# Kernel optimization log

Hardware: AMD Instinct MI355X
Metric: run time of the kernel (lower is better)

Reference implementation:

```python
import jax, jax.numpy as jnp
import numpy as np

N, C, H, W = 4, 256, 32, 32
NH = 2                      # att_nhead
HD = C // NH                # 128 per-head dim
MAX_DIS = 7
WS = 2 * MAX_DIS + 1        # 15 window side
WW = WS * WS                # 225 window positions
T = (C / NH) ** 0.5


def _gather_idx(h, w):
    # idx[wpos, m]: flat index into zero-padded (h+14, w+14) grid of the
    # neighbor at window offset wpos for query pixel m (== F.unfold semantics)
    pw = w + 2 * MAX_DIS
    dy, dx = np.meshgrid(np.arange(WS), np.arange(WS), indexing='ij')
    ys, xs = np.meshgrid(np.arange(h), np.arange(w), indexing='ij')
    idx = (dy.reshape(-1, 1) + ys.reshape(1, -1)) * pw + (dx.reshape(-1, 1) + xs.reshape(1, -1))
    return jnp.asarray(idx, dtype=jnp.int32)  # [WW, h*w]


def setup_inputs() -> dict:
    key = jax.random.key(0)
    ks = jax.random.split(key, 14)
    s = 0.02
    return {
        'q': jax.random.normal(ks[0], (N, C, H, W), jnp.float32),
        'k': jax.random.normal(ks[1], (N, C, H, W), jnp.float32),
        'v': jax.random.normal(ks[2], (N, C, H, W), jnp.float32),
        'Wq': jax.random.normal(ks[3], (C, C), jnp.float32) * s,
        'bq': jnp.zeros((C,), jnp.float32),
        'Wk': jax.random.normal(ks[4], (C, C), jnp.float32) * s,
        'bk': jnp.zeros((C,), jnp.float32),
        'Wv': jax.random.normal(ks[5], (C, C), jnp.float32) * s,
        'bv': jnp.zeros((C,), jnp.float32),
        'Wrel': jax.random.normal(ks[6], (NH, WW, HD), jnp.float32) * s,   # grouped 1x1 conv
        'brel': jnp.zeros((NH * WW,), jnp.float32),
        'V_bias': jax.random.normal(ks[7], (NH, HD, WW), jnp.float32) * s,
        'Wfc': jax.random.normal(ks[8], (C, C), jnp.float32) * s,
        'bfc': jnp.zeros((C,), jnp.float32),
    }


def _conv1x1(x, Wt, b):
    return jnp.einsum('nchw,dc->ndhw', x, Wt) + b[None, :, None, None]


def reference(q, k, v, Wq, bq, Wk, bk, Wv, bv, Wrel, brel, V_bias, Wfc, bfc):
    n, c, h, w = q.shape
    hw = h * w
    idx = _gather_idx(h, w)                                   # [WW, hw]
    pad = ((0, 0), (0, 0), (0, 0), (MAX_DIS, MAX_DIS), (MAX_DIS, MAX_DIS))

    q = _conv1x1(q, Wq, bq)
    k = _conv1x1(k, Wk, bk)
    v = _conv1x1(v, Wv, bv)

    # grouped 1x1 conv: relative position logits, [n, NH, WW, hw]
    rel = jnp.einsum('ngcxy,gwc->ngwxy', q.reshape(n, NH, HD, h, w), Wrel)
    rel = rel + brel.reshape(NH, WW)[None, :, :, None, None]
    rel = rel.reshape(n, NH, WW, hw)

    qs = (q / T).reshape(n, NH, HD, hw)

    # unfold K via zero-pad + gather: [n, NH, HD, WW, hw]
    k_pad = jnp.pad(k.reshape(n, NH, HD, h, w), pad).reshape(n, NH, HD, -1)
    k_un = k_pad[..., idx]
    qk = jnp.einsum('ngcm,ngcwm->ngwm', qs, k_un) + rel

    # boundary mask: neighbor inside the original image
    valid = jnp.pad(jnp.ones((h, w), jnp.float32), MAX_DIS).reshape(-1)[idx] > 0
    qk = jnp.where(valid[None, None], qk, jnp.float32(-1e8))
    attn = jax.nn.softmax(qk, axis=2)                         # over window positions

    agg_bias = jnp.einsum('ngwm,gcw->mngc', attn, V_bias).reshape(hw, n, c)

    # local2global scatter + dense einsum == gather of zero-padded V
    v_pad = jnp.pad(v.reshape(n, NH, HD, h, w), pad).reshape(n, NH, HD, -1)
    v_un = v_pad[..., idx]                                    # [n, NH, HD, WW, hw]
    agg_value = jnp.einsum('ngwm,ngcwm->mngc', attn, v_un).reshape(hw, n, c)

    out = (agg_value + agg_bias) @ Wfc.T + bfc                # [hw, n, c]
    return out
```

## Files before the change

kernel.cpp:

```cpp
#include <hip/hip_runtime.h>
#include <math.h>


typedef __attribute__((ext_vector_type(8))) short short8;
typedef __attribute__((ext_vector_type(4))) float floatx4;

__device__ __forceinline__ short f2bf(float f) {
    unsigned u = __float_as_uint(f);
    unsigned r = (u + 0x7fffu + ((u >> 16) & 1u)) >> 16;
    return (short)r;
}
__device__ __forceinline__ float bf2f(short s) {
    return __uint_as_float(((unsigned)(unsigned short)s) << 16);
}

__global__ __launch_bounds__(256)
void prep(const float* __restrict__ Wq, const float* __restrict__ Wk,
          const float* __restrict__ Wv,
          short* __restrict__ Whi, short* __restrict__ Wlo)
{
    const int tid = threadIdx.x;
    const int sub = tid >> 6, lane = tid & 63;
    const int n16 = lane & 15, quad = lane >> 4;
    const int u = blockIdx.x * 4 + sub;

    const int sel = u >> 7, rem = u & 127;
    const int dt = rem >> 3, kc = rem & 7;
    const float* W = (sel == 0 ? Wq : sel == 1 ? Wk : Wv);
    const int d = dt * 16 + n16, cb = kc * 32 + quad * 8;
    float4 w0 = *(const float4*)&W[(long)d * 256 + cb];
    float4 w1 = *(const float4*)&W[(long)d * 256 + cb + 4];
    float f[8] = {w0.x, w0.y, w0.z, w0.w, w1.x, w1.y, w1.z, w1.w};
    short8 h8, l8;
#pragma unroll
    for (int j = 0; j < 8; ++j) {
        short hb = f2bf(f[j]);
        h8[j] = hb;
        l8[j] = f2bf(f[j] - bf2f(hb));
    }
    long off = (long)sel * 65536 + (((long)(dt * 8 + kc) * 64) + lane) * 8;
    *(short8*)(Whi + off) = h8;
    *(short8*)(Wlo + off) = l8;
}

__global__ __launch_bounds__(256)
void mfma_proj(const float* __restrict__ q, const float* __restrict__ k,
               const float* __restrict__ v,
               const float* __restrict__ Wfc, const float* __restrict__ Wrel,
               const float* __restrict__ Vb,
               short* Whi, short* Wlo,
               const float* __restrict__ bq, const float* __restrict__ bk,
               const float* __restrict__ bv,
               short* __restrict__ qhi, short* __restrict__ qlo,
               short* __restrict__ khi, short* __restrict__ klo,
               short* __restrict__ vhi, short* __restrict__ vlo,
               short* __restrict__ Wrh, short* __restrict__ Wrl,
               short* __restrict__ Vbh, short* __restrict__ Vbl)
{
    __shared__ float st[256 * 17];
    const int tid = threadIdx.x;
    const int wave = tid >> 6, lane = tid & 63;
    const int n16 = lane & 15, quad = lane >> 4;
    const int z = blockIdx.y;

    if (z == 12) {
#pragma unroll
        for (int s = 0; s < 2; ++s) {
            const int u = blockIdx.x * 8 + wave * 2 + s;
            if (u < 128) {
                const int dt = u >> 3, kc = u & 7;
                const int d = dt * 16 + n16, cb = kc * 32 + quad * 8;
                float4 w0 = *(const float4*)&Wfc[(long)d * 256 + cb];
                float4 w1 = *(const float4*)&Wfc[(long)d * 256 + cb + 4];
                float f[8] = {w0.x, w0.y, w0.z, w0.w, w1.x, w1.y, w1.z, w1.w};
                short8 h8, l8;
#pragma unroll
                for (int j = 0; j < 8; ++j) {
                    short hb = f2bf(f[j]);
                    h8[j] = hb;
                    l8[j] = f2bf(f[j] - bf2f(hb));
                }
                long off = (long)3 * 65536 + (((long)(dt * 8 + kc) * 64) + lane) * 8;
                *(short8*)(Whi + off) = h8;
                *(short8*)(Wlo + off) = l8;
            } else if (u < 248) {
                const int t = u - 128;
                const int g = t / 60, r = t - g * 60;
                const int wt = r >> 2, kc = r & 3;
                const int w = wt * 16 + n16;
                const int cb = kc * 32 + quad * 8;
                float f[8] = {0.f, 0.f, 0.f, 0.f, 0.f, 0.f, 0.f, 0.f};
                if (w < 225) {
                    float4 w0 = *(const float4*)&Wrel[(long)(g * 225 + w) * 128 + cb];
                    float4 w1 = *(const float4*)&Wrel[(long)(g * 225 + w) * 128 + cb + 4];
                    f[0] = w0.x; f[1] = w0.y; f[2] = w0.z; f[3] = w0.w;
                    f[4] = w1.x; f[5] = w1.y; f[6] = w1.z; f[7] = w1.w;
                }
                short8 h8, l8;
#pragma unroll
                for (int j = 0; j < 8; ++j) {
                    short hb = f2bf(f[j]);
                    h8[j] = hb;
                    l8[j] = f2bf(f[j] - bf2f(hb));
                }
                long off = (long)g * 30720 + (((long)(wt * 4 + kc) * 64) + lane) * 8;
                *(short8*)(Wrh + off) = h8;
                *(short8*)(Wrl + off) = l8;
            } else if (u < 376) {
                const int t = u - 248;
                const int g = t >> 6, r = t & 63;
                const int dt = r >> 3, wk = r & 7;
                const int ch = dt * 16 + n16;
                const int w0 = wk * 32 + quad * 8;
                float f[8];
#pragma unroll
                for (int j = 0; j < 8; ++j) {
                    int w = w0 + j;
                    f[j] = (w < 225) ? Vb[(long)(g * 128 + ch) * 225 + w] : 0.f;
                }
                short8 h8, l8;
#pragma unroll
                for (int j = 0; j < 8; ++j) {
                    short hb = f2bf(f[j]);
                    h8[j] = hb;
                    l8[j] = f2bf(f[j] - bf2f(hb));
                }
                long off = (((long)(g * 128 + ch)) << 8) + w0;
                *(short8*)(Vbh + off) = h8;
                *(short8*)(Vbl + off) = l8;
            }
        }
        return;
    }

    const int mt16 = blockIdx.x;
    const int sel = z >> 2, batch = z & 3;
    const float* X = (sel == 0 ? q : sel == 1 ? k : v) + ((long)batch << 18);

    {
#pragma unroll
        for (int p = 0; p < 4; ++p) {
            const int c = p * 64 + (tid >> 2), m4 = (tid & 3) * 4;
            float4 a = *(const float4*)&X[((long)c << 10) + mt16 * 16 + m4];
            float* d = &st[c * 17 + m4];
            d[0] = a.x; d[1] = a.y; d[2] = a.z; d[3] = a.w;
        }
    }

    const float* bias = (sel == 0 ? bq : sel == 1 ? bk : bv);
    float bbv[4][4];
#pragma unroll
    for (int i = 0; i < 4; ++i) {
        float4 b4 = *(const float4*)&bias[(wave * 4 + i) * 16 + quad * 4];
        bbv[i][0] = b4.x; bbv[i][1] = b4.y; bbv[i][2] = b4.z; bbv[i][3] = b4.w;
    }
    __syncthreads();

    floatx4 acc[4] = {{0.f,0.f,0.f,0.f},{0.f,0.f,0.f,0.f},
                      {0.f,0.f,0.f,0.f},{0.f,0.f,0.f,0.f}};
    const long abase = (long)sel * 65536 + (long)lane * 8;
#pragma unroll
    for (int kc = 0; kc < 8; ++kc) {
        short8 bh, bl;
        const float* col = &st[(kc * 32 + quad * 8) * 17 + n16];
#pragma unroll
        for (int j = 0; j < 8; ++j) {
            float f = col[j * 17];
            short hb = f2bf(f);
            bh[j] = hb;
            bl[j] = f2bf(f - bf2f(hb));
        }
#pragma unroll
        for (int i = 0; i < 4; ++i) {
            const int dt = wave * 4 + i;
            short8 ahi = *(const short8*)(Whi + abase + (long)(dt * 8 + kc) * 512);
            short8 alo = *(const short8*)(Wlo + abase + (long)(dt * 8 + kc) * 512);
            acc[i] = __builtin_amdgcn_mfma_f32_16x16x32_bf16(ahi, bh, acc[i], 0, 0, 0);
            acc[i] = __builtin_amdgcn_mfma_f32_16x16x32_bf16(ahi, bl, acc[i], 0, 0, 0);
            acc[i] = __builtin_amdgcn_mfma_f32_16x16x32_bf16(alo, bh, acc[i], 0, 0, 0);
        }
    }

    __syncthreads();
    float* tile = st;
#pragma unroll
    for (int i = 0; i < 4; ++i) {
        const int dt = wave * 4 + i;
#pragma unroll
        for (int r = 0; r < 4; ++r)
            tile[n16 * 257 + dt * 16 + quad * 4 + r] = acc[i][r] + bbv[i][r];
    }
    __syncthreads();

    if (sel == 2) {
        const int gg = tid >> 7, chp = tid & 127;
        const int yq = mt16 >> 1, xb = (mt16 & 1) * 16;
        short8 h0, h1, l0, l1;
#pragma unroll
        for (int j = 0; j < 8; ++j) {
            float f0 = tile[j * 257 + tid];
            float f1 = tile[(j + 8) * 257 + tid];
            short hb0 = f2bf(f0), hb1 = f2bf(f1);
            h0[j] = hb0; l0[j] = f2bf(f0 - bf2f(hb0));
            h1[j] = hb1; l1[j] = f2bf(f1 - bf2f(hb1));
        }
        long o = ((long)((batch * 2 + gg) * 128 + chp) * 32 + yq) * 48 + 8 + xb;
        *(short8*)(vhi + o) = h0;
        *(short8*)(vhi + o + 8) = h1;
        *(short8*)(vlo + o) = l0;
        *(short8*)(vlo + o + 8) = l1;
        const int prow = mt16 >> 1, side = mt16 & 1;
        long po = ((long)((batch * 2 + gg) * 128 + chp) * 32 + prow) * 48 + side * 40;
        short8 zz = {0,0,0,0,0,0,0,0};
        *(short8*)(vhi + po) = zz;
        *(short8*)(vlo + po) = zz;
        return;
    }

    const float scale = (sel == 1) ? 0.08838834764831845f : 1.0f;
    const int m_l = tid >> 4, c16 = (tid & 15) * 16;
    const int m = mt16 * 16 + m_l;
    short* oh = sel ? khi : qhi;
    short* ol = sel ? klo : qlo;
#pragma unroll
    for (int half = 0; half < 2; ++half) {
        const int cg = c16 + half * 8;
        short8 h8, l8;
#pragma unroll
        for (int j = 0; j < 8; ++j) {
            float f = tile[m_l * 257 + cg + j] * scale;
            short hb = f2bf(f);
            h8[j] = hb;
            l8[j] = f2bf(f - bf2f(hb));
        }
        const int g = cg >> 7, ch = cg & 127;
        const long base = (((long)(batch * 2 + g) << 10) + m) * 128 + ch;
        *(short8*)(oh + base) = h8;
        *(short8*)(ol + base) = l8;
    }
}

__global__ __launch_bounds__(512)
void scores_pv(const short* __restrict__ qhi, const short* __restrict__ qlo,
               const short* __restrict__ khi, const short* __restrict__ klo,
               const short* __restrict__ Wrh, const short* __restrict__ Wrl,
               const float* __restrict__ brel,
               const short* __restrict__ vhi, const short* __restrict__ vlo,
               const short* __restrict__ Vbh, const short* __restrict__ Vbl,
               short* __restrict__ AGhi, short* __restrict__ AGlo)
{
    __shared__ __align__(16) float qk[16 * 241];
    __shared__ __align__(16) short pah[16 * 264];
    __shared__ __align__(16) short pal[16 * 264];
    __shared__ float invl[16];

    const int tid = threadIdx.x;
    const int wave = tid >> 6, lane = tid & 63;
    const int lin = blockIdx.x;
    const int bz  = lin & 7;
    const int yy  = lin >> 3;
    const int y   = yy >> 1;
    const int xt  = yy & 1;
    const int g = bz & 1;
    const int x0 = xt * 16;

    const int n16 = lane & 15, quad = lane >> 4;
    const long qbase = (((long)bz << 10) + y * 32 + x0 + n16) * 128 + quad * 8;
    short8 a_hi[4], a_lo[4];
#pragma unroll
    for (int ch = 0; ch < 4; ++ch) {
        a_hi[ch] = *(const short8*)(qhi + qbase + ch * 32);
        a_lo[ch] = *(const short8*)(qlo + qbase + ch * 32);
    }

    for (int wt = wave; wt < 15; wt += 8) {
        const short* Ah = Wrh + (long)g * 30720 + ((long)(wt * 4) * 64 + lane) * 8;
        const short* Al = Wrl + (long)g * 30720 + ((long)(wt * 4) * 64 + lane) * 8;
        floatx4 racc = {0.f, 0.f, 0.f, 0.f};
#pragma unroll
        for (int kc = 0; kc < 4; ++kc) {
            short8 whh = *(const short8*)(Ah + kc * 512);
            short8 wll = *(const short8*)(Al + kc * 512);
            racc = __builtin_amdgcn_mfma_f32_16x16x32_bf16(whh, a_hi[kc], racc, 0, 0, 0);
            racc = __builtin_amdgcn_mfma_f32_16x16x32_bf16(whh, a_lo[kc], racc, 0, 0, 0);
            racc = __builtin_amdgcn_mfma_f32_16x16x32_bf16(wll, a_hi[kc], racc, 0, 0, 0);
        }
#pragma unroll
        for (int r = 0; r < 4; ++r) {
            int w = wt * 16 + quad * 4 + r;
            if (w < 225) {
                int dy = w / 15, dx = w - dy * 15;
                int hy = y + dy - 7, hx = x0 + n16 + dx - 7;
                bool valid = (hy >= 0) && (hy < 32) && (hx >= 0) && (hx < 32);
                qk[n16 * 241 + dy * 16 + dx] =
                    valid ? (racc[r] + brel[g * 225 + w]) : -1e8f;
            }
        }
    }
    if (tid < 256) {
        int px = tid >> 4, p = tid & 15;
        int slot = (p < 15) ? (p * 16 + 15) : 240;
        qk[px * 241 + slot] = -1e8f;
    }
    __syncthreads();

    for (int dy = wave; dy < 15; dy += 8) {
        const int ky = y + dy - 7;
        if (ky < 0 || ky > 31) continue;
#pragma unroll
        for (int kxt = 0; kxt < 2; ++kxt) {
            const int kxg = x0 - 8 + kxt * 16 + n16;
            const long kb = (((long)bz << 10) + ky * 32 + kxg) * 128 + quad * 8;
            floatx4 acc = {0.f, 0.f, 0.f, 0.f};
#pragma unroll
            for (int ch = 0; ch < 4; ++ch) {
                short8 b_hi = *(const short8*)(khi + kb + ch * 32);
                short8 b_lo = *(const short8*)(klo + kb + ch * 32);
                acc = __builtin_amdgcn_mfma_f32_16x16x32_bf16(a_hi[ch], b_hi, acc, 0, 0, 0);
                acc = __builtin_amdgcn_mfma_f32_16x16x32_bf16(a_hi[ch], b_lo, acc, 0, 0, 0);
                acc = __builtin_amdgcn_mfma_f32_16x16x32_bf16(a_lo[ch], b_hi, acc, 0, 0, 0);
            }
            if (kxg >= 0 && kxg < 32) {
#pragma unroll
                for (int r = 0; r < 4; ++r) {
                    int m = quad * 4 + r;
                    int dx = kxg - (x0 + m) + 7;
                    if (dx >= 0 && dx < 15) {
                        int s = m * 241 + dy * 16 + dx;
                        qk[s] = qk[s] + acc[r];
                    }
                }
            }
        }
    }
    __syncthreads();

    {
        int px = tid >> 5, s = tid & 31;
        float mx = -3.0e38f;
        for (int w = s; w < 240; w += 32) mx = fmaxf(mx, qk[px * 241 + w]);
#pragma unroll
        for (int msk = 16; msk; msk >>= 1) mx = fmaxf(mx, __shfl_xor(mx, msk));
        float sum = 0.f;
        for (int w = s; w < 240; w += 32) {
            float p = __expf(qk[px * 241 + w] - mx);
            qk[px * 241 + w] = p;
            sum += p;
        }
#pragma unroll
        for (int msk = 16; msk; msk >>= 1) sum += __shfl_xor(sum, msk);
        if (s == 0) invl[px] = 1.0f / sum;
    }
    __syncthreads();

    for (int e = tid; e < 4096; e += 512) {
        int px = e >> 8, w = e & 255;
        float p = 0.f;
        if (w < 225) {
            int dy2 = w / 15, dx2 = w - dy2 * 15;
            p = qk[px * 241 + dy2 * 16 + dx2] * invl[px];
        }
        short hb = f2bf(p);
        pah[px * 264 + w] = hb;
        pal[px * 264 + w] = f2bf(p - bf2f(hb));
    }
    __syncthreads();

    floatx4 acc = {0.f, 0.f, 0.f, 0.f};
    const int ch0 = wave * 16;

#pragma unroll
    for (int wk = 0; wk < 8; ++wk) {
        short8 pa_h = *(const short8*)&pah[n16 * 264 + wk * 32 + quad * 8];
        short8 pa_l = *(const short8*)&pal[n16 * 264 + wk * 32 + quad * 8];
        const long vb0 = (((long)(g * 128 + ch0 + n16)) << 8) + wk * 32 + quad * 8;
        short8 b0h = *(const short8*)(Vbh + vb0);
        short8 b0l = *(const short8*)(Vbl + vb0);
        acc = __builtin_amdgcn_mfma_f32_16x16x32_bf16(pa_h, b0h, acc, 0, 0, 0);
        acc = __builtin_amdgcn_mfma_f32_16x16x32_bf16(pa_h, b0l, acc, 0, 0, 0);
        acc = __builtin_amdgcn_mfma_f32_16x16x32_bf16(pa_l, b0h, acc, 0, 0, 0);
    }

    for (int dy = 0; dy < 15; ++dy) {
        const int ky = y + dy - 7;
        if (ky < 0 || ky > 31) continue;
        short8 bnd_h, bnd_l;
        const int rowoff = n16 * 264 + dy * 15 - n16 - 1;
#pragma unroll
        for (int j = 0; j < 8; ++j) {
            int kk = quad * 8 + j;
            int dx = kk - n16 - 1;
            bool valid = (unsigned)dx < 15u;
            int idx = valid ? (rowoff + kk) : 0;
            short vh = pah[idx];
            short vl = pal[idx];
            bnd_h[j] = valid ? vh : (short)0;
            bnd_l[j] = valid ? vl : (short)0;
        }
        const long v0o = (((long)((bz * 128 + ch0 + n16)) * 32 + ky)) * 48 + x0 + quad * 8;
        short8 v0h = *(const short8*)(vhi + v0o);
        short8 v0l = *(const short8*)(vlo + v0o);
        acc = __builtin_amdgcn_mfma_f32_16x16x32_bf16(bnd_h, v0h, acc, 0, 0, 0);
        acc = __builtin_amdgcn_mfma_f32_16x16x32_bf16(bnd_h, v0l, acc, 0, 0, 0);
        acc = __builtin_amdgcn_mfma_f32_16x16x32_bf16(bnd_l, v0h, acc, 0, 0, 0);
    }

    float* tile = qk;
    {
        const int cb = ch0 + n16;
#pragma unroll
        for (int r = 0; r < 4; ++r)
            tile[(quad * 4 + r) * 133 + cb] = acc[r];
    }
    __syncthreads();

    const int sub = tid >> 6;
    if (sub < 4) {
        short8 h8, l8;
#pragma unroll
        for (int j = 0; j < 8; ++j) {
            float f = tile[n16 * 133 + sub * 32 + quad * 8 + j];
            short hb = f2bf(f);
            h8[j] = hb;
            l8[j] = f2bf(f - bf2f(hb));
        }
        const int n = bz >> 1;
        const int mt16 = y * 2 + xt;
        const int kc = g * 4 + sub;
        long off = (long)n * 262144 + (((long)(mt16 * 8 + kc) * 64) + lane) * 8;
        *(short8*)(AGhi + off) = h8;
        *(short8*)(AGlo + off) = l8;
    }
}

__global__ __launch_bounds__(256)
void mfma_fc(const short* __restrict__ Ahi, const short* __restrict__ Alo,
             const short* __restrict__ Whi, const short* __restrict__ Wlo,
             const float* __restrict__ bfc, float* __restrict__ out)
{
    __shared__ float tile[16 * 68];
    const int tid = threadIdx.x;
    const int wave = tid >> 6, lane = tid & 63;
    const int n16 = lane & 15, quad = lane >> 4;
    const int mt16 = blockIdx.x, db = blockIdx.y, nz = blockIdx.z;
    const int dt = db * 4 + wave;

    const short* Ah = Whi + (long)3 * 65536 + ((long)(dt * 8) * 64 + lane) * 8;
    const short* Al = Wlo + (long)3 * 65536 + ((long)(dt * 8) * 64 + lane) * 8;
    const short* Bh = Ahi + (long)nz * 262144;
    const short* Bl = Alo + (long)nz * 262144;

    float4 bv4 = *(const float4*)&bfc[dt * 16 + quad * 4];
    float bb[4] = {bv4.x, bv4.y, bv4.z, bv4.w};

    floatx4 acc = {0.f, 0.f, 0.f, 0.f};
#pragma unroll
    for (int kc = 0; kc < 8; ++kc) {
        short8 ahi = *(const short8*)(Ah + kc * 512);
        short8 alo = *(const short8*)(Al + kc * 512);
        long bo = ((long)(mt16 * 8 + kc) * 64 + lane) * 8;
        short8 bh = *(const short8*)(Bh + bo);
        short8 bl = *(const short8*)(Bl + bo);
        acc = __builtin_amdgcn_mfma_f32_16x16x32_bf16(ahi, bh, acc, 0, 0, 0);
        acc = __builtin_amdgcn_mfma_f32_16x16x32_bf16(ahi, bl, acc, 0, 0, 0);
        acc = __builtin_amdgcn_mfma_f32_16x16x32_bf16(alo, bh, acc, 0, 0, 0);
    }

    const int dl = wave * 16 + quad * 4;
#pragma unroll
    for (int r = 0; r < 4; ++r)
        tile[n16 * 68 + dl + r] = acc[r] + bb[r];
    __syncthreads();

    const int mm = tid >> 4, d4 = (tid & 15) * 4;
    float4 o4 = *(const float4*)&tile[mm * 68 + d4];
    *(float4*)&out[(long)(mt16 * 16 + mm) * 1024 + nz * 256 + db * 64 + d4] = o4;
}

extern "C" void kernel_launch(void* const* d_in, const int* in_sizes, int n_in,
                              void* d_out, int out_size, void* d_ws, size_t ws_size,
                              hipStream_t stream)
{
    const float* q    = (const float*)d_in[0];
    const float* k    = (const float*)d_in[1];
    const float* v    = (const float*)d_in[2];
    const float* Wq   = (const float*)d_in[3];
    const float* bq   = (const float*)d_in[4];
    const float* Wk   = (const float*)d_in[5];
    const float* bk   = (const float*)d_in[6];
    const float* Wv   = (const float*)d_in[7];
    const float* bv   = (const float*)d_in[8];
    const float* Wrel = (const float*)d_in[9];
    const float* brel = (const float*)d_in[10];
    const float* Vb   = (const float*)d_in[11];
    const float* Wfc  = (const float*)d_in[12];
    const float* bfc  = (const float*)d_in[13];
    float* out = (float*)d_out;

    float* ws   = (float*)d_ws;
    short* vhi  = (short*)(ws + 2097152);
    short* vlo  = (short*)(ws + 2883584);
    short* Vbh  = (short*)(ws + 4718592);
    short* Vbl  = (short*)(ws + 4751360);
    short* qhi  = (short*)(ws + 6561792);
    short* qlo  = (short*)(ws + 7086080);
    short* khi  = (short*)(ws + 7610368);
    short* klo  = (short*)(ws + 8134656);
    short* Whi  = (short*)(ws + 11804672);
    short* Wlo  = (short*)(ws + 11935744);
    short* AGhi = (short*)(ws + 12066816);
    short* AGlo = (short*)(ws + 12591104);
    short* Wrh  = (short*)(ws + 13115392);
    short* Wrl  = (short*)(ws + 13146112);

    prep<<<dim3(96), dim3(256), 0, stream>>>(Wq, Wk, Wv, Whi, Wlo);

    mfma_proj<<<dim3(64, 13), dim3(256), 0, stream>>>(q, k, v, Wfc, Wrel, Vb,
                                                      Whi, Wlo,
                                                      bq, bk, bv,
                                                      qhi, qlo, khi, klo,
                                                      vhi, vlo,
                                                      Wrh, Wrl, Vbh, Vbl);

    scores_pv<<<dim3(512), dim3(512), 0, stream>>>(qhi, qlo, khi, klo,
                                                   Wrh, Wrl, brel,
                                                   vhi, vlo, Vbh, Vbl,
                                                   AGhi, AGlo);

    mfma_fc<<<dim3(64, 4, 4), dim3(256), 0, stream>>>(AGhi, AGlo, Whi, Wlo,
                                                      bfc, out);
}
```

Measured before the change: 154.2 us.

## Fuse output FC projection into scores_pv via last-block atomic counter

Removes the separate mfma_fc launch. Each pair of blocks covering both heads of a 16-pixel tile increments an atomic counter, and the second one to finish reads the complete aggregated tile and runs the 256-wide FC projection with MFMA before writing the output. Counters are zeroed in the prep kernel. This saves a kernel launch and the gap between kernels, at the cost of a tail of serial FC work in the winning blocks and a dependence on threadfence ordering.

```diff
diff --git a/kernel.cpp b/kernel.cpp
--- a/kernel.cpp
+++ b/kernel.cpp
@@ -17,9 +17,12 @@
 __global__ __launch_bounds__(256)
 void prep(const float* __restrict__ Wq, const float* __restrict__ Wk,
           const float* __restrict__ Wv,
-          short* __restrict__ Whi, short* __restrict__ Wlo)
+          short* __restrict__ Whi, short* __restrict__ Wlo,
+          int* __restrict__ cnt)
 {
     const int tid = threadIdx.x;
+    if (blockIdx.x == 0) cnt[tid] = 0;
+
     const int sub = tid >> 6, lane = tid & 63;
     const int n16 = lane & 15, quad = lane >> 4;
     const int u = blockIdx.x * 4 + sub;
@@ -247,12 +250,16 @@
                const float* __restrict__ brel,
                const short* __restrict__ vhi, const short* __restrict__ vlo,
                const short* __restrict__ Vbh, const short* __restrict__ Vbl,
-               short* __restrict__ AGhi, short* __restrict__ AGlo)
+               const short* __restrict__ Whi, const short* __restrict__ Wlo,
+               short* __restrict__ AGhi, short* __restrict__ AGlo,
+               const float* __restrict__ bfc, float* __restrict__ out,
+               int* __restrict__ cnt)
 {
     __shared__ __align__(16) float qk[16 * 241];
     __shared__ __align__(16) short pah[16 * 264];
     __shared__ __align__(16) short pal[16 * 264];
     __shared__ float invl[16];
+    __shared__ int winner;
 
     const int tid = threadIdx.x;
     const int wave = tid >> 6, lane = tid & 63;
@@ -414,6 +421,7 @@
     }
     __syncthreads();
 
+    const int nn = bz >> 1;
     const int sub = tid >> 6;
     if (sub < 4) {
         short8 h8, l8;
@@ -424,57 +432,52 @@
             h8[j] = hb;
             l8[j] = f2bf(f - bf2f(hb));
         }
-        const int n = bz >> 1;
-        const int mt16 = y * 2 + xt;
         const int kc = g * 4 + sub;
-        long off = (long)n * 262144 + (((long)(mt16 * 8 + kc) * 64) + lane) * 8;
+        long off = (long)nn * 262144 + (((long)(yy * 8 + kc) * 64) + lane) * 8;
         *(short8*)(AGhi + off) = h8;
         *(short8*)(AGlo + off) = l8;
     }
-}
-
-__global__ __launch_bounds__(256)
-void mfma_fc(const short* __restrict__ Ahi, const short* __restrict__ Alo,
-             const short* __restrict__ Whi, const short* __restrict__ Wlo,
-             const float* __restrict__ bfc, float* __restrict__ out)
-{
-    __shared__ float tile[16 * 68];
-    const int tid = threadIdx.x;
-    const int wave = tid >> 6, lane = tid & 63;
-    const int n16 = lane & 15, quad = lane >> 4;
-    const int mt16 = blockIdx.x, db = blockIdx.y, nz = blockIdx.z;
-    const int dt = db * 4 + wave;
-
-    const short* Ah = Whi + (long)3 * 65536 + ((long)(dt * 8) * 64 + lane) * 8;
-    const short* Al = Wlo + (long)3 * 65536 + ((long)(dt * 8) * 64 + lane) * 8;
-    const short* Bh = Ahi + (long)nz * 262144;
-    const short* Bl = Alo + (long)nz * 262144;
-
-    float4 bv4 = *(const float4*)&bfc[dt * 16 + quad * 4];
-    float bb[4] = {bv4.x, bv4.y, bv4.z, bv4.w};
-
-    floatx4 acc = {0.f, 0.f, 0.f, 0.f};
+
+    __threadfence();
+    __syncthreads();
+    if (tid == 0) {
+        winner = (atomicAdd(&cnt[nn * 64 + yy], 1) == 1) ? 1 : 0;
+    }
+    __syncthreads();
+    if (!winner) return;
+    __threadfence();
+
+    const short* Bh = AGhi + (long)nn * 262144;
+    const short* Bl = AGlo + (long)nn * 262144;
+    const long wbase = (long)3 * 65536 + (long)lane * 8;
+    const int dt0 = wave * 2, dt1 = wave * 2 + 1;
+    floatx4 fa0 = {0.f, 0.f, 0.f, 0.f};
+    floatx4 fa1 = {0.f, 0.f, 0.f, 0.f};
 #pragma unroll
     for (int kc = 0; kc < 8; ++kc) {
-        short8 ahi = *(const short8*)(Ah + kc * 512);
-        short8 alo = *(const short8*)(Al + kc * 512);
-        long bo = ((long)(mt16 * 8 + kc) * 64 + lane) * 8;
+        const long bo = ((long)(yy * 8 + kc) * 64 + lane) * 8;
         short8 bh = *(const short8*)(Bh + bo);
         short8 bl = *(const short8*)(Bl + bo);
-        acc = __builtin_amdgcn_mfma_f32_16x16x32_bf16(ahi, bh, acc, 0, 0, 0);
-        acc = __builtin_amdgcn_mfma_f32_16x16x32_bf16(ahi, bl, acc, 0, 0, 0);
-        acc = __builtin_amdgcn_mfma_f32_16x16x32_bf16(alo, bh, acc, 0, 0, 0);
-    }
-
-    const int dl = wave * 16 + quad * 4;
-#pragma unroll
-    for (int r = 0; r < 4; ++r)
-        tile[n16 * 68 + dl + r] = acc[r] + bb[r];
-    __syncthreads();
-
-    const int mm = tid >> 4, d4 = (tid & 15) * 4;
-    float4 o4 = *(const float4*)&tile[mm * 68 + d4];
-    *(float4*)&out[(long)(mt16 * 16 + mm) * 1024 + nz * 256 + db * 64 + d4] = o4;
+        short8 a0h = *(const short8*)(Whi + wbase + (long)(dt0 * 8 + kc) * 512);
+        short8 a0l = *(const short8*)(Wlo + wbase + (long)(dt0 * 8 + kc) * 512);
+        fa0 = __builtin_amdgcn_mfma_f32_16x16x32_bf16(a0h, bh, fa0, 0, 0, 0);
+        fa0 = __builtin_amdgcn_mfma_f32_16x16x32_bf16(a0h, bl, fa0, 0, 0, 0);
+        fa0 = __builtin_amdgcn_mfma_f32_16x16x32_bf16(a0l, bh, fa0, 0, 0, 0);
+        short8 a1h = *(const short8*)(Whi + wbase + (long)(dt1 * 8 + kc) * 512);
+        short8 a1l = *(const short8*)(Wlo + wbase + (long)(dt1 * 8 + kc) * 512);
+        fa1 = __builtin_amdgcn_mfma_f32_16x16x32_bf16(a1h, bh, fa1, 0, 0, 0);
+        fa1 = __builtin_amdgcn_mfma_f32_16x16x32_bf16(a1h, bl, fa1, 0, 0, 0);
+        fa1 = __builtin_amdgcn_mfma_f32_16x16x32_bf16(a1l, bh, fa1, 0, 0, 0);
+    }
+    {
+        const long ob = (long)(yy * 16 + n16) * 1024 + nn * 256;
+        float4 b0 = *(const float4*)&bfc[dt0 * 16 + quad * 4];
+        float4 o0 = {fa0[0] + b0.x, fa0[1] + b0.y, fa0[2] + b0.z, fa0[3] + b0.w};
+        *(float4*)&out[ob + dt0 * 16 + quad * 4] = o0;
+        float4 b1 = *(const float4*)&bfc[dt1 * 16 + quad * 4];
+        float4 o1 = {fa1[0] + b1.x, fa1[1] + b1.y, fa1[2] + b1.z, fa1[3] + b1.w};
+        *(float4*)&out[ob + dt1 * 16 + quad * 4] = o1;
+    }
 }
 
 extern "C" void kernel_launch(void* const* d_in, const int* in_sizes, int n_in,
@@ -512,8 +515,9 @@
     short* AGlo = (short*)(ws + 12591104);
     short* Wrh  = (short*)(ws + 13115392);
     short* Wrl  = (short*)(ws + 13146112);
-
-    prep<<<dim3(96), dim3(256), 0, stream>>>(Wq, Wk, Wv, Whi, Wlo);
+    int*   cnt  = (int*)(ws + 13180928);
+
+    prep<<<dim3(96), dim3(256), 0, stream>>>(Wq, Wk, Wv, Whi, Wlo, cnt);
 
     mfma_proj<<<dim3(64, 13), dim3(256), 0, stream>>>(q, k, v, Wfc, Wrel, Vb,
                                                       Whi, Wlo,
@@ -525,8 +529,7 @@
     scores_pv<<<dim3(512), dim3(512), 0, stream>>>(qhi, qlo, khi, klo,
                                                    Wrh, Wrl, brel,
                                                    vhi, vlo, Vbh, Vbl,
-                                                   AGhi, AGlo);
-
-    mfma_fc<<<dim3(64, 4, 4), dim3(256), 0, stream>>>(AGhi, AGlo, Whi, Wlo,
-                                                      bfc, out);
+                                                   Whi, Wlo,
+                                                   AGhi, AGlo,
+                                                   bfc, out, cnt);
 }
```

Result: slower. 341.0 us (+121.2%).
